# Optimization experiments

Hardware: AMD Instinct MI355X
Metric: run time of the kernel (lower is better)

## Reference

```python
import jax, jax.numpy as jnp
import numpy as np

D_MODEL = 512
NHEAD = 8


def setup_inputs() -> dict:
    key = jax.random.key(0)
    k0, k1, k2 = jax.random.split(key, 3)
    s = 1.0 / np.sqrt(D_MODEL)  # torch default uniform init bound (xavier-ish)
    return {
        "x": jax.random.normal(k0, (2, 4096, D_MODEL), dtype=jnp.float32),
        "in_proj_w": jax.random.uniform(k1, (3 * D_MODEL, D_MODEL), jnp.float32, -s, s),
        "in_proj_b": jnp.zeros((3 * D_MODEL,), jnp.float32),
        "out_proj_w": jax.random.uniform(k2, (D_MODEL, D_MODEL), jnp.float32, -s, s),
        "out_proj_b": jnp.zeros((D_MODEL,), jnp.float32),
        "window_size": 128,
    }


def reference(x, in_proj_w, in_proj_b, out_proj_w, out_proj_b, window_size):
    # Faithful to nn.MultiheadAttention (eval mode, dropout inactive).
    # NOTE: PyTorch bool attn_mask: True = disallowed. The module sets True
    # INSIDE the window, so in-window positions are masked OUT.
    B, S, D = x.shape
    H = NHEAD
    hd = D // H

    qkv = x @ in_proj_w.T + in_proj_b                      # [B,S,3D]
    q, k, v = jnp.split(qkv, 3, axis=-1)
    q = q.reshape(B, S, H, hd).transpose(0, 2, 1, 3)       # [B,H,S,hd]
    k = k.reshape(B, S, H, hd).transpose(0, 2, 1, 3)
    v = v.reshape(B, S, H, hd).transpose(0, 2, 1, 3)

    scores = jnp.einsum('bhqd,bhkd->bhqk', q, k) / jnp.sqrt(jnp.float32(hd))

    idx = jnp.arange(S)
    in_window = jnp.abs(idx[:, None] - idx[None, :]) <= window_size  # [S,S]
    scores = jnp.where(in_window, -jnp.inf, scores)

    attn = jax.nn.softmax(scores, axis=-1)                 # [B,H,S,S]
    ctx = jnp.einsum('bhqk,bhkd->bhqd', attn, v)           # [B,H,S,hd]
    ctx = ctx.transpose(0, 2, 1, 3).reshape(B, S, D)       # [B,S,D]
    return ctx @ out_proj_w.T + out_proj_b
```

## Files before the change

kernel.cpp:

```cpp
#include <hip/hip_runtime.h>
#include <hip/hip_bf16.h>

typedef unsigned short u16;
typedef __bf16 bf16x8 __attribute__((ext_vector_type(8)));
typedef float f32x4 __attribute__((ext_vector_type(4)));

__device__ __forceinline__ f32x4 mfma16(bf16x8 a, bf16x8 b, f32x4 c) {
    return __builtin_amdgcn_mfma_f32_16x16x32_bf16(a, b, c, 0, 0, 0);
}

__device__ __forceinline__ u16 f2b(float x) {
    union { float f; unsigned u; } a; a.f = x;
    unsigned r = a.u + 0x7fffu + ((a.u >> 16) & 1u);
    return (u16)(r >> 16);
}
__device__ __forceinline__ unsigned f2b2(float a, float b) {
    union { __hip_bfloat162 h; unsigned u; } cv;
    cv.h = __float22bfloat162_rn(make_float2(a, b));
    return cv.u;
}
__device__ __forceinline__ void async16(const u16* g, u16* l) {
    __builtin_amdgcn_global_load_lds((const __attribute__((address_space(1))) unsigned int*)g,
                                     (__attribute__((address_space(3))) unsigned int*)l, 16, 0, 0);
}

#define NX  (8192 * 512)
#define NWQ (1536 * 512)
#define NWO (512 * 512)
__global__ __launch_bounds__(256) void k_cast_all(const float* __restrict__ x,
                                                  const float* __restrict__ wq,
                                                  const float* __restrict__ wo,
                                                  u16* __restrict__ xb,
                                                  u16* __restrict__ wqb,
                                                  u16* __restrict__ wob) {
    int i = (blockIdx.x * 256 + threadIdx.x) * 4;
    const float* s; u16* d; int off;
    if (i < NX)            { s = x;  d = xb;  off = i; }
    else if (i < NX + NWQ) { s = wq; d = wqb; off = i - NX; }
    else                   { s = wo; d = wob; off = i - NX - NWQ; }
    float4 f = *(const float4*)&s[off];
    uint2 o = make_uint2(f2b2(f.x, f.y), f2b2(f.z, f.w));
    *(uint2*)&d[off] = o;
}

__global__ __launch_bounds__(256, 3) void k_gemm_qkv(const u16* __restrict__ xb,
                                                     const u16* __restrict__ wb,
                                                     const float* __restrict__ bias,
                                                     u16* __restrict__ qkvout) {
    __shared__ u16 AL[2][4096];
    __shared__ u16 WL[2][4096];
    const int tid = threadIdx.x;
    const int w = tid >> 6, lane = tid & 63, l15 = lane & 15, quad = lane >> 4;
    const int mb = blockIdx.x * 128, nb = blockIdx.y * 128;

    f32x4 acc[2][8];
#pragma unroll
    for (int i = 0; i < 2; i++)
#pragma unroll
        for (int j = 0; j < 8; j++) acc[i][j] = (f32x4){0.f, 0.f, 0.f, 0.f};

    const u16* agp = xb + (size_t)(mb + w * 32 + (lane >> 2)) * 512 + (lane & 3) * 8;
    const u16* wgp = wb + (size_t)(nb + w * 32 + (lane >> 2)) * 512 + (lane & 3) * 8;
    const int ldst = w * 1024 + lane * 8;

    async16(agp, &AL[0][ldst]);
    async16(agp + 16 * 512, &AL[0][ldst + 512]);
    async16(wgp, &WL[0][ldst]);
    async16(wgp + 16 * 512, &WL[0][ldst + 512]);
    __syncthreads();
    int p = 0;
    for (int ks = 0; ks < 16; ks++) {
        if (ks < 15) {
            int k0n = (ks + 1) * 32;
            async16(agp + k0n, &AL[p ^ 1][ldst]);
            async16(agp + 16 * 512 + k0n, &AL[p ^ 1][ldst + 512]);
            async16(wgp + k0n, &WL[p ^ 1][ldst]);
            async16(wgp + 16 * 512 + k0n, &WL[p ^ 1][ldst + 512]);
        }
        bf16x8 a0 = *(const bf16x8*)&AL[p][(w * 32 + l15) * 32 + quad * 8];
        bf16x8 a1 = *(const bf16x8*)&AL[p][(w * 32 + 16 + l15) * 32 + quad * 8];
#pragma unroll
        for (int nt = 0; nt < 8; nt++) {
            bf16x8 bfr = *(const bf16x8*)&WL[p][(nt * 16 + l15) * 32 + quad * 8];
            acc[0][nt] = mfma16(a0, bfr, acc[0][nt]);
            acc[1][nt] = mfma16(a1, bfr, acc[1][nt]);
        }
        if (ks < 15) { __syncthreads(); p ^= 1; }
    }
    const int seg = nb >> 9;
    u16* obase = qkvout + (size_t)seg * (16ull * 4096 * 64);
    if (seg == 0) {
        const float sc = 0.125f * 1.44269504088896340736f;
#pragma unroll
        for (int mt = 0; mt < 2; mt++)
#pragma unroll
            for (int nt = 0; nt < 8; nt++) {
                int dcol = nb + nt * 16 + l15;
                int hh = (dcol >> 6) & 7, dloc = dcol & 63;
                float bs = bias[dcol];
#pragma unroll
                for (int r = 0; r < 4; r++) {
                    int m = mb + w * 32 + mt * 16 + quad * 4 + r;
                    float vv = (acc[mt][nt][r] + bs) * sc;
                    int b = m >> 12, s = m & 4095;
                    obase[((size_t)((b * 8 + hh) * 4096 + s)) * 64 + dloc] = f2b(vv);
                }
            }
    } else if (seg == 1) {
#pragma unroll
        for (int mt = 0; mt < 2; mt++)
#pragma unroll
            for (int nt = 0; nt < 8; nt++) {
                int dcol = nb + nt * 16 + l15;
                int hh = (dcol >> 6) & 7, d = dcol & 63;
                int h2 = d >> 5, qk = (d >> 3) & 3, j = d & 7;
                float bs = bias[dcol];
                int m0 = mb + w * 32 + mt * 16 + quad * 4;
                int b = m0 >> 12, s0 = m0 & 4095;
                int kt = s0 >> 6, ksx = s0 & 63;
                int kg2 = ksx >> 5, rem = ksx & 31;
                int t2 = (rem >> 2) & 1, lb = (rem >> 3) * 4;
                size_t base = ((((((size_t)(b * 8 + hh) * 64 + kt) * 2 + kg2) * 2 + t2) * 2 + h2) * 4 + qk) * 16 + lb;
#pragma unroll
                for (int r = 0; r < 4; r++)
                    obase[(base + r) * 8 + j] = f2b(acc[mt][nt][r] + bs);
            }
    } else {
#pragma unroll
        for (int mt = 0; mt < 2; mt++)
#pragma unroll
            for (int nt = 0; nt < 8; nt++) {
                int c = nb + nt * 16 + l15;
                int hh = (c >> 6) & 7, d = c & 63;
                int mbv = d >> 4, l15v = d & 15;
                float bs = bias[c];
                int m0 = mb + w * 32 + mt * 16 + quad * 4;
                int b = m0 >> 12, si = m0 & 4095;
                int kt = si >> 6, ksx = si & 63;
                int kg2 = ksx >> 5, qv = (ksx >> 3) & 3, j0 = ksx & 7;
                uint2 o = make_uint2(f2b2(acc[mt][nt][0] + bs, acc[mt][nt][1] + bs),
                                     f2b2(acc[mt][nt][2] + bs, acc[mt][nt][3] + bs));
                size_t F = (((((size_t)(b * 8 + hh) * 64 + kt) * 2 + kg2) * 4 + mbv) * 4 + qv) * 16 + l15v;
                *(uint2*)&obase[F * 8 + j0] = o;
            }
    }
}

__global__ __launch_bounds__(256, 2) void k_attn(const u16* __restrict__ qg,
                                                 const u16* __restrict__ kfg,
                                                 const u16* __restrict__ vfg,
                                                 u16* __restrict__ ctx,
                                                 const int* __restrict__ win) {
    __shared__ u16 KL[2][4096];
    __shared__ u16 VL[2][4096];
    const int tid = threadIdx.x;
    const int w = tid >> 6, lane = tid & 63, l15 = lane & 15, quad = lane >> 4;
    const int bh = blockIdx.y;
    const int qb0 = blockIdx.x * 128;
    const int qb0w = qb0 + w * 32;
    const int W = win[0];
    const size_t bhb = (size_t)bh * 4096 * 64;

    bf16x8 qf[2][2];
#pragma unroll
    for (int g = 0; g < 2; g++) {
        const u16* qrow = &qg[bhb + (size_t)(qb0w + g * 16 + l15) * 64];
        qf[g][0] = *(const bf16x8*)&qrow[quad * 8];
        qf[g][1] = *(const bf16x8*)&qrow[32 + quad * 8];
    }
    bf16x8 ones8;
    {
        u16 v = (l15 == 0) ? (u16)0x3F80 : (u16)0;
        union { u16 a[8]; bf16x8 b; } c;
#pragma unroll
        for (int i = 0; i < 8; i++) c.a[i] = v;
        ones8 = c.b;
    }

    f32x4 O[2][4];
#pragma unroll
    for (int g = 0; g < 2; g++)
#pragma unroll
        for (int mb = 0; mb < 4; mb++) O[g][mb] = (f32x4){0.f, 0.f, 0.f, 0.f};
    f32x4 O1[2] = {(f32x4){0.f, 0.f, 0.f, 0.f}, (f32x4){0.f, 0.f, 0.f, 0.f}};

    const u16* kbase = kfg + bhb;
    const u16* vbase = vfg + bhb;
    const int soff = w * 1024 + lane * 8;

    auto skip = [&](int kb) { return max(qb0 + 127 - kb, kb + 63 - qb0) <= W; };
    int kb = 0;
    while (kb < 4096 && skip(kb)) kb += 64;
    {
        const u16* kt_p = kbase + (size_t)(kb >> 6) * 4096;
        const u16* vt_p = vbase + (size_t)(kb >> 6) * 4096;
        async16(kt_p + soff, &KL[0][soff]);
        async16(kt_p + soff + 512, &KL[0][soff + 512]);
        async16(vt_p + soff, &VL[0][soff]);
        async16(vt_p + soff + 512, &VL[0][soff + 512]);
    }
    __syncthreads();
    int p = 0;
    while (kb < 4096) {
        int kb_next = kb + 64;
        while (kb_next < 4096 && skip(kb_next)) kb_next += 64;
        if (kb_next < 4096) {
            const u16* kt_p = kbase + (size_t)(kb_next >> 6) * 4096;
            const u16* vt_p = vbase + (size_t)(kb_next >> 6) * 4096;
            async16(kt_p + soff, &KL[p ^ 1][soff]);
            async16(kt_p + soff + 512, &KL[p ^ 1][soff + 512]);
            async16(vt_p + soff, &VL[p ^ 1][soff]);
            async16(vt_p + soff + 512, &VL[p ^ 1][soff + 512]);
        }
        const bool partial = (kb + 63 >= qb0 - W) && (kb <= qb0 + 127 + W);
        bf16x8 kf[2][2][2];
#pragma unroll
        for (int kg = 0; kg < 2; kg++)
#pragma unroll
            for (int t = 0; t < 2; t++)
#pragma unroll
                for (int h = 0; h < 2; h++)
                    kf[kg][t][h] = *(const bf16x8*)&KL[p][((((kg * 2 + t) * 2 + h) * 4 + quad) * 16 + l15) * 8];
        bf16x8 vfr[2][4];
#pragma unroll
        for (int kg = 0; kg < 2; kg++)
#pragma unroll
            for (int mb = 0; mb < 4; mb++)
                vfr[kg][mb] = *(const bf16x8*)&VL[p][(((kg * 4 + mb) * 4 + quad) * 16 + l15) * 8];

        f32x4 C[2][2][2];
#pragma unroll
        for (int g = 0; g < 2; g++)
#pragma unroll
            for (int kg = 0; kg < 2; kg++)
#pragma unroll
                for (int t = 0; t < 2; t++) {
                    f32x4 z = (f32x4){0.f, 0.f, 0.f, 0.f};
                    C[g][kg][t] = mfma16(kf[kg][t][0], qf[g][0], z);
                    C[g][kg][t] = mfma16(kf[kg][t][1], qf[g][1], C[g][kg][t]);
                }
        bf16x8 pb[2][2];
        if (!partial) {
#pragma unroll
            for (int g = 0; g < 2; g++)
#pragma unroll
                for (int kg = 0; kg < 2; kg++) {
                    float p0 = __builtin_amdgcn_exp2f(C[g][kg][0][0]);
                    float p1 = __builtin_amdgcn_exp2f(C[g][kg][0][1]);
                    float p2 = __builtin_amdgcn_exp2f(C[g][kg][0][2]);
                    float p3 = __builtin_amdgcn_exp2f(C[g][kg][0][3]);
                    float p4 = __builtin_amdgcn_exp2f(C[g][kg][1][0]);
                    float p5 = __builtin_amdgcn_exp2f(C[g][kg][1][1]);
                    float p6 = __builtin_amdgcn_exp2f(C[g][kg][1][2]);
                    float p7 = __builtin_amdgcn_exp2f(C[g][kg][1][3]);
                    union { uint4 u; bf16x8 v; } pk;
                    pk.u = make_uint4(f2b2(p0, p1), f2b2(p2, p3), f2b2(p4, p5), f2b2(p6, p7));
                    pb[g][kg] = pk.v;
                }
        } else {
#pragma unroll
            for (int g = 0; g < 2; g++) {
                int qr = qb0w + g * 16 + l15;
#pragma unroll
                for (int kg = 0; kg < 2; kg++) {
                    float pv[8];
#pragma unroll
                    for (int t = 0; t < 2; t++)
#pragma unroll
                        for (int r = 0; r < 4; r++) {
                            int key = kb + kg * 32 + 8 * quad + 4 * t + r;
                            int dd = qr - key; dd = dd < 0 ? -dd : dd;
                            pv[t * 4 + r] = (dd <= W) ? 0.f
                                          : __builtin_amdgcn_exp2f(C[g][kg][t][r]);
                        }
                    union { uint4 u; bf16x8 v; } pk;
                    pk.u = make_uint4(f2b2(pv[0], pv[1]), f2b2(pv[2], pv[3]),
                                      f2b2(pv[4], pv[5]), f2b2(pv[6], pv[7]));
                    pb[g][kg] = pk.v;
                }
            }
        }
#pragma unroll
        for (int kg = 0; kg < 2; kg++)
#pragma unroll
            for (int g = 0; g < 2; g++) {
#pragma unroll
                for (int mb = 0; mb < 4; mb++)
                    O[g][mb] = mfma16(vfr[kg][mb], pb[g][kg], O[g][mb]);
                O1[g] = mfma16(ones8, pb[g][kg], O1[g]);
            }
        if (kb_next < 4096) { __syncthreads(); p ^= 1; }
        kb = kb_next;
    }
    int b = bh >> 3, h = bh & 7;
#pragma unroll
    for (int g = 0; g < 2; g++) {
        float ls = __shfl(O1[g][0], l15);
        float inv = 1.0f / ls;
        int qr = qb0w + g * 16 + l15;
        size_t rowoff = ((size_t)(b * 4096 + qr)) * 512 + h * 64;
#pragma unroll
        for (int mb = 0; mb < 4; mb++) {
            uint2 o = make_uint2(f2b2(O[g][mb][0] * inv, O[g][mb][1] * inv),
                                 f2b2(O[g][mb][2] * inv, O[g][mb][3] * inv));
            *(uint2*)&ctx[rowoff + mb * 16 + quad * 4] = o;
        }
    }
}

__global__ __launch_bounds__(256, 2) void k_gemm_out(const u16* __restrict__ ab,
                                                     const u16* __restrict__ wb,
                                                     const float* __restrict__ bias,
                                                     float* __restrict__ out) {
    __shared__ u16 AL[2][4096];
    __shared__ u16 WL[2][2048];
    const int tid = threadIdx.x;
    const int w = tid >> 6, lane = tid & 63, l15 = lane & 15, quad = lane >> 4;
    const int mb = blockIdx.x * 128, nb = blockIdx.y * 64;

    f32x4 acc[2][4];
#pragma unroll
    for (int i = 0; i < 2; i++)
#pragma unroll
        for (int j = 0; j < 4; j++) acc[i][j] = (f32x4){0.f, 0.f, 0.f, 0.f};

    const u16* agp = ab + (size_t)(mb + w * 32 + (lane >> 2)) * 512 + (lane & 3) * 8;
    const u16* wgp = wb + (size_t)(nb + w * 16 + (lane >> 2)) * 512 + (lane & 3) * 8;
    const int ldstA = w * 1024 + lane * 8;
    const int ldstW = w * 512 + lane * 8;

    async16(agp, &AL[0][ldstA]);
    async16(agp + 16 * 512, &AL[0][ldstA + 512]);
    async16(wgp, &WL[0][ldstW]);
    __syncthreads();
    int p = 0;
    for (int ks = 0; ks < 16; ks++) {
        if (ks < 15) {
            int k0n = (ks + 1) * 32;
            async16(agp + k0n, &AL[p ^ 1][ldstA]);
            async16(agp + 16 * 512 + k0n, &AL[p ^ 1][ldstA + 512]);
            async16(wgp + k0n, &WL[p ^ 1][ldstW]);
        }
        bf16x8 a0 = *(const bf16x8*)&AL[p][(w * 32 + l15) * 32 + quad * 8];
        bf16x8 a1 = *(const bf16x8*)&AL[p][(w * 32 + 16 + l15) * 32 + quad * 8];
#pragma unroll
        for (int nt = 0; nt < 4; nt++) {
            bf16x8 bfr = *(const bf16x8*)&WL[p][(nt * 16 + l15) * 32 + quad * 8];
            acc[0][nt] = mfma16(a0, bfr, acc[0][nt]);
            acc[1][nt] = mfma16(a1, bfr, acc[1][nt]);
        }
        if (ks < 15) { __syncthreads(); p ^= 1; }
    }
#pragma unroll
    for (int mt = 0; mt < 2; mt++)
#pragma unroll
        for (int nt = 0; nt < 4; nt++) {
            int n = nb + nt * 16 + l15;
            float bs = bias[n];
#pragma unroll
            for (int r = 0; r < 4; r++) {
                int m = mb + w * 32 + mt * 16 + quad * 4 + r;
                out[(size_t)m * 512 + n] = acc[mt][nt][r] + bs;
            }
        }
}

extern "C" void kernel_launch(void* const* d_in, const int* in_sizes, int n_in,
                              void* d_out, int out_size, void* d_ws, size_t ws_size,
                              hipStream_t stream) {
    const float* x    = (const float*)d_in[0];
    const float* wqkv = (const float*)d_in[1];
    const float* bqkv = (const float*)d_in[2];
    const float* wout = (const float*)d_in[3];
    const float* bout = (const float*)d_in[4];
    const int*   win  = (const int*)d_in[5];
    float* out = (float*)d_out;

    u16* xb    = (u16*)d_ws;
    u16* wqkvb = xb    + 8192ull * 512;
    u16* woutb = wqkvb + 1536ull * 512;
    u16* qkvb  = woutb + 512ull * 512;
    u16* ctxb  = qkvb  + 3ull * 16 * 4096 * 64;

    k_cast_all<<<5120, 256, 0, stream>>>(x, wqkv, wout, xb, wqkvb, woutb);
    k_gemm_qkv<<<dim3(64, 12), 256, 0, stream>>>(xb, wqkvb, bqkv, qkvb);
    k_attn<<<dim3(32, 16), 256, 0, stream>>>(qkvb, qkvb + 16ull * 4096 * 64,
                                             qkvb + 32ull * 4096 * 64, ctxb, win);
    k_gemm_out<<<dim3(64, 8), 256, 0, stream>>>(ctxb, woutb, bout, out);
}
```

Before: 198.7 us.

## Use single-wave attention blocks with register-prefetched V and LDS-staged K

The attention kernel now launches one 64-thread wave per block, each handling 32 query rows, instead of four waves sharing a 128-row block. This removes block-wide barriers. K tiles are double-buffered in LDS through async loads, while V fragments are prefetched straight into registers for the next tile, with an explicit waitcnt standing in for __syncthreads. The tighter per-wave skip window lets each wave skip more fully masked tiles. In exchange, each K/V tile is loaded four times as often, raising global/L2 traffic, and register pressure goes up from the V prefetch.

```diff
diff --git a/kernel.cpp b/kernel.cpp
--- a/kernel.cpp
+++ b/kernel.cpp
@@ -146,25 +146,23 @@
     }
 }
 
-__global__ __launch_bounds__(256, 2) void k_attn(const u16* __restrict__ qg,
-                                                 const u16* __restrict__ kfg,
-                                                 const u16* __restrict__ vfg,
-                                                 u16* __restrict__ ctx,
-                                                 const int* __restrict__ win) {
-    __shared__ u16 KL[2][4096];
-    __shared__ u16 VL[2][4096];
-    const int tid = threadIdx.x;
-    const int w = tid >> 6, lane = tid & 63, l15 = lane & 15, quad = lane >> 4;
+__global__ __launch_bounds__(64, 2) void k_attn(const u16* __restrict__ qg,
+                                                const u16* __restrict__ kfg,
+                                                const u16* __restrict__ vfg,
+                                                u16* __restrict__ ctx,
+                                                const int* __restrict__ win) {
+    __shared__ u16 KP[2][4096];
+    const int lane = threadIdx.x & 63;
+    const int l15 = lane & 15, quad = lane >> 4;
     const int bh = blockIdx.y;
-    const int qb0 = blockIdx.x * 128;
-    const int qb0w = qb0 + w * 32;
+    const int qb0 = blockIdx.x * 32;
     const int W = win[0];
     const size_t bhb = (size_t)bh * 4096 * 64;
 
     bf16x8 qf[2][2];
 #pragma unroll
     for (int g = 0; g < 2; g++) {
-        const u16* qrow = &qg[bhb + (size_t)(qb0w + g * 16 + l15) * 64];
+        const u16* qrow = &qg[bhb + (size_t)(qb0 + g * 16 + l15) * 64];
         qf[g][0] = *(const bf16x8*)&qrow[quad * 8];
         qf[g][1] = *(const bf16x8*)&qrow[32 + quad * 8];
     }
@@ -184,35 +182,28 @@
         for (int mb = 0; mb < 4; mb++) O[g][mb] = (f32x4){0.f, 0.f, 0.f, 0.f};
     f32x4 O1[2] = {(f32x4){0.f, 0.f, 0.f, 0.f}, (f32x4){0.f, 0.f, 0.f, 0.f}};
 
-    const u16* kbase = kfg + bhb;
-    const u16* vbase = vfg + bhb;
-    const int soff = w * 1024 + lane * 8;
-
-    auto skip = [&](int kb) { return max(qb0 + 127 - kb, kb + 63 - qb0) <= W; };
-    int kb = 0;
-    while (kb < 4096 && skip(kb)) kb += 64;
+    const u16* kbase = kfg + bhb + lane * 8;
+    const u16* vbase = vfg + bhb + lane * 8;
+
+    auto skip = [&](int kb) { return max(qb0 + 31 - kb, kb + 63 - qb0) <= W; };
+    auto nextk = [&](int kb) { while (kb < 4096 && skip(kb)) kb += 64; return kb; };
+
+    bf16x8 vn[8];
+    int kb = nextk(0);
     {
-        const u16* kt_p = kbase + (size_t)(kb >> 6) * 4096;
-        const u16* vt_p = vbase + (size_t)(kb >> 6) * 4096;
-        async16(kt_p + soff, &KL[0][soff]);
-        async16(kt_p + soff + 512, &KL[0][soff + 512]);
-        async16(vt_p + soff, &VL[0][soff]);
-        async16(vt_p + soff + 512, &VL[0][soff + 512]);
-    }
-    __syncthreads();
+        const u16* kp = kbase + (size_t)(kb >> 6) * 4096;
+        const u16* vp = vbase + (size_t)(kb >> 6) * 4096;
+#pragma unroll
+        for (int i = 0; i < 8; i++) async16(kp + i * 512, &KP[0][i * 512 + lane * 8]);
+#pragma unroll
+        for (int f = 0; f < 8; f++) vn[f] = *(const bf16x8*)(vp + f * 512);
+    }
     int p = 0;
     while (kb < 4096) {
-        int kb_next = kb + 64;
-        while (kb_next < 4096 && skip(kb_next)) kb_next += 64;
-        if (kb_next < 4096) {
-            const u16* kt_p = kbase + (size_t)(kb_next >> 6) * 4096;
-            const u16* vt_p = vbase + (size_t)(kb_next >> 6) * 4096;
-            async16(kt_p + soff, &KL[p ^ 1][soff]);
-            async16(kt_p + soff + 512, &KL[p ^ 1][soff + 512]);
-            async16(vt_p + soff, &VL[p ^ 1][soff]);
-            async16(vt_p + soff + 512, &VL[p ^ 1][soff + 512]);
-        }
-        const bool partial = (kb + 63 >= qb0 - W) && (kb <= qb0 + 127 + W);
+        __builtin_amdgcn_s_waitcnt(0x0F70);
+        bf16x8 vc[8];
+#pragma unroll
+        for (int f = 0; f < 8; f++) vc[f] = vn[f];
         bf16x8 kf[2][2][2];
 #pragma unroll
         for (int kg = 0; kg < 2; kg++)
@@ -220,14 +211,17 @@
             for (int t = 0; t < 2; t++)
 #pragma unroll
                 for (int h = 0; h < 2; h++)
-                    kf[kg][t][h] = *(const bf16x8*)&KL[p][((((kg * 2 + t) * 2 + h) * 4 + quad) * 16 + l15) * 8];
-        bf16x8 vfr[2][4];
-#pragma unroll
-        for (int kg = 0; kg < 2; kg++)
-#pragma unroll
-            for (int mb = 0; mb < 4; mb++)
-                vfr[kg][mb] = *(const bf16x8*)&VL[p][(((kg * 4 + mb) * 4 + quad) * 16 + l15) * 8];
-
+                    kf[kg][t][h] = *(const bf16x8*)&KP[p][((((kg * 2 + t) * 2 + h) * 4 + quad) * 16 + l15) * 8];
+        int kn = nextk(kb + 64);
+        if (kn < 4096) {
+            const u16* kp = kbase + (size_t)(kn >> 6) * 4096;
+            const u16* vp = vbase + (size_t)(kn >> 6) * 4096;
+#pragma unroll
+            for (int i = 0; i < 8; i++) async16(kp + i * 512, &KP[p ^ 1][i * 512 + lane * 8]);
+#pragma unroll
+            for (int f = 0; f < 8; f++) vn[f] = *(const bf16x8*)(vp + f * 512);
+        }
+        const bool partial = (kb + 63 >= qb0 - W) && (kb <= qb0 + 31 + W);
         f32x4 C[2][2][2];
 #pragma unroll
         for (int g = 0; g < 2; g++)
@@ -260,7 +254,7 @@
         } else {
 #pragma unroll
             for (int g = 0; g < 2; g++) {
-                int qr = qb0w + g * 16 + l15;
+                int qr = qb0 + g * 16 + l15;
 #pragma unroll
                 for (int kg = 0; kg < 2; kg++) {
                     float pv[8];
@@ -286,18 +280,18 @@
             for (int g = 0; g < 2; g++) {
 #pragma unroll
                 for (int mb = 0; mb < 4; mb++)
-                    O[g][mb] = mfma16(vfr[kg][mb], pb[g][kg], O[g][mb]);
+                    O[g][mb] = mfma16(vc[kg * 4 + mb], pb[g][kg], O[g][mb]);
                 O1[g] = mfma16(ones8, pb[g][kg], O1[g]);
             }
-        if (kb_next < 4096) { __syncthreads(); p ^= 1; }
-        kb = kb_next;
+        p ^= 1;
+        kb = kn;
     }
     int b = bh >> 3, h = bh & 7;
 #pragma unroll
     for (int g = 0; g < 2; g++) {
         float ls = __shfl(O1[g][0], l15);
         float inv = 1.0f / ls;
-        int qr = qb0w + g * 16 + l15;
+        int qr = qb0 + g * 16 + l15;
         size_t rowoff = ((size_t)(b * 4096 + qr)) * 512 + h * 64;
 #pragma unroll
         for (int mb = 0; mb < 4; mb++) {
@@ -384,7 +378,7 @@
 
     k_cast_all<<<5120, 256, 0, stream>>>(x, wqkv, wout, xb, wqkvb, woutb);
     k_gemm_qkv<<<dim3(64, 12), 256, 0, stream>>>(xb, wqkvb, bqkv, qkvb);
-    k_attn<<<dim3(32, 16), 256, 0, stream>>>(qkvb, qkvb + 16ull * 4096 * 64,
+    k_attn<<<dim3(128, 16), 64, 0, stream>>>(qkvb, qkvb + 16ull * 4096 * 64,
                                              qkvb + 32ull * 4096 * 64, ctxb, win);
     k_gemm_out<<<dim3(64, 8), 256, 0, stream>>>(ctxb, woutb, bout, out);
 }
```

Result: slower. 213.5 us (+7.5%).

## Split attention key range across two wave groups per block and merge partials

Applied to the files above, without the earlier changes.

The attention kernel now launches 512 threads per block. Two groups of four waves each process half of the non-skipped key tiles for the same 128-query block, each with its own double-buffered LDS staging. At the end, group 1 writes its partial output and row sums to shared memory and group 0 adds them and normalizes. The aim is more parallelism on the serial key loop, since the grid of only 512 blocks underfills the GPU. The cost is doubled LDS, an extra reduction through shared memory, and block-wide barriers that now also wait on the other group.

```diff
diff --git a/kernel.cpp b/kernel.cpp
--- a/kernel.cpp
+++ b/kernel.cpp
@@ -146,15 +146,16 @@
     }
 }
 
-__global__ __launch_bounds__(256, 2) void k_attn(const u16* __restrict__ qg,
+__global__ __launch_bounds__(512, 4) void k_attn(const u16* __restrict__ qg,
                                                  const u16* __restrict__ kfg,
                                                  const u16* __restrict__ vfg,
                                                  u16* __restrict__ ctx,
                                                  const int* __restrict__ win) {
-    __shared__ u16 KL[2][4096];
-    __shared__ u16 VL[2][4096];
+    __shared__ u16 KL[2][2][4096];
+    __shared__ u16 VL[2][2][4096];
     const int tid = threadIdx.x;
-    const int w = tid >> 6, lane = tid & 63, l15 = lane & 15, quad = lane >> 4;
+    const int wid = tid >> 6, grp = wid >> 2, w = wid & 3;
+    const int lane = tid & 63, l15 = lane & 15, quad = lane >> 4;
     const int bh = blockIdx.y;
     const int qb0 = blockIdx.x * 128;
     const int qb0w = qb0 + w * 32;
@@ -186,124 +187,153 @@
 
     const u16* kbase = kfg + bhb;
     const u16* vbase = vfg + bhb;
-    const int soff = w * 1024 + lane * 8;
-
-    auto skip = [&](int kb) { return max(qb0 + 127 - kb, kb + 63 - qb0) <= W; };
-    int kb = 0;
-    while (kb < 4096 && skip(kb)) kb += 64;
-    {
-        const u16* kt_p = kbase + (size_t)(kb >> 6) * 4096;
-        const u16* vt_p = vbase + (size_t)(kb >> 6) * 4096;
-        async16(kt_p + soff, &KL[0][soff]);
-        async16(kt_p + soff + 512, &KL[0][soff + 512]);
-        async16(vt_p + soff, &VL[0][soff]);
-        async16(vt_p + soff + 512, &VL[0][soff + 512]);
-    }
+    const int tidg = tid & 255;
+    const int soff = (tidg >> 6) * 1024 + lane * 8;
+
+    int a = qb0 + 127 - W;
+    int T_lo = (a <= 0) ? 0 : ((a + 63) >> 6);
+    int b2 = qb0 + W - 63;
+    int T_hi = (b2 < 0) ? -1 : (b2 >> 6);
+    if (T_hi > 63) T_hi = 63;
+    if (T_lo > 63) T_lo = 64;
+    int cnt = T_hi - T_lo + 1; if (cnt < 0) cnt = 0;
+    const int nvalid = 64 - cnt;
+    const int n0 = (nvalid + 1) >> 1, n1 = nvalid - n0;
+    const int base = grp ? n0 : 0;
+    const int mycnt = grp ? n1 : n0;
+    auto tileof = [&](int idx) { return ((idx < T_lo) ? idx : idx + cnt) << 6; };
+    auto stage = [&](int idx, int buf) {
+        int kt = tileof(idx) >> 6;
+        const u16* kt_p = kbase + (size_t)kt * 4096;
+        const u16* vt_p = vbase + (size_t)kt * 4096;
+        async16(kt_p + soff, &KL[grp][buf][soff]);
+        async16(kt_p + soff + 512, &KL[grp][buf][soff + 512]);
+        async16(vt_p + soff, &VL[grp][buf][soff]);
+        async16(vt_p + soff + 512, &VL[grp][buf][soff + 512]);
+    };
+
+    if (mycnt > 0) stage(base, 0);
     __syncthreads();
     int p = 0;
-    while (kb < 4096) {
-        int kb_next = kb + 64;
-        while (kb_next < 4096 && skip(kb_next)) kb_next += 64;
-        if (kb_next < 4096) {
-            const u16* kt_p = kbase + (size_t)(kb_next >> 6) * 4096;
-            const u16* vt_p = vbase + (size_t)(kb_next >> 6) * 4096;
-            async16(kt_p + soff, &KL[p ^ 1][soff]);
-            async16(kt_p + soff + 512, &KL[p ^ 1][soff + 512]);
-            async16(vt_p + soff, &VL[p ^ 1][soff]);
-            async16(vt_p + soff + 512, &VL[p ^ 1][soff + 512]);
-        }
-        const bool partial = (kb + 63 >= qb0 - W) && (kb <= qb0 + 127 + W);
-        bf16x8 kf[2][2][2];
-#pragma unroll
-        for (int kg = 0; kg < 2; kg++)
-#pragma unroll
-            for (int t = 0; t < 2; t++)
-#pragma unroll
-                for (int h = 0; h < 2; h++)
-                    kf[kg][t][h] = *(const bf16x8*)&KL[p][((((kg * 2 + t) * 2 + h) * 4 + quad) * 16 + l15) * 8];
-        bf16x8 vfr[2][4];
-#pragma unroll
-        for (int kg = 0; kg < 2; kg++)
+    for (int i = 0; i < n0; i++) {
+        if (i + 1 < mycnt) stage(base + i + 1, p ^ 1);
+        if (i < mycnt) {
+            const int kb = tileof(base + i);
+            const bool partial = (kb + 63 >= qb0 - W) && (kb <= qb0 + 127 + W);
+            bf16x8 kf[2][2][2];
+#pragma unroll
+            for (int kg = 0; kg < 2; kg++)
+#pragma unroll
+                for (int t = 0; t < 2; t++)
+#pragma unroll
+                    for (int h = 0; h < 2; h++)
+                        kf[kg][t][h] = *(const bf16x8*)&KL[grp][p][((((kg * 2 + t) * 2 + h) * 4 + quad) * 16 + l15) * 8];
+            bf16x8 vfr[2][4];
+#pragma unroll
+            for (int kg = 0; kg < 2; kg++)
+#pragma unroll
+                for (int mb = 0; mb < 4; mb++)
+                    vfr[kg][mb] = *(const bf16x8*)&VL[grp][p][(((kg * 4 + mb) * 4 + quad) * 16 + l15) * 8];
+
+            f32x4 C[2][2][2];
+#pragma unroll
+            for (int g = 0; g < 2; g++)
+#pragma unroll
+                for (int kg = 0; kg < 2; kg++)
+#pragma unroll
+                    for (int t = 0; t < 2; t++) {
+                        f32x4 z = (f32x4){0.f, 0.f, 0.f, 0.f};
+                        C[g][kg][t] = mfma16(kf[kg][t][0], qf[g][0], z);
+                        C[g][kg][t] = mfma16(kf[kg][t][1], qf[g][1], C[g][kg][t]);
+                    }
+            bf16x8 pb[2][2];
+            if (!partial) {
+#pragma unroll
+                for (int g = 0; g < 2; g++)
+#pragma unroll
+                    for (int kg = 0; kg < 2; kg++) {
+                        float p0 = __builtin_amdgcn_exp2f(C[g][kg][0][0]);
+                        float p1 = __builtin_amdgcn_exp2f(C[g][kg][0][1]);
+                        float p2 = __builtin_amdgcn_exp2f(C[g][kg][0][2]);
+                        float p3 = __builtin_amdgcn_exp2f(C[g][kg][0][3]);
+                        float p4 = __builtin_amdgcn_exp2f(C[g][kg][1][0]);
+                        float p5 = __builtin_amdgcn_exp2f(C[g][kg][1][1]);
+                        float p6 = __builtin_amdgcn_exp2f(C[g][kg][1][2]);
+                        float p7 = __builtin_amdgcn_exp2f(C[g][kg][1][3]);
+                        union { uint4 u; bf16x8 v; } pk;
+                        pk.u = make_uint4(f2b2(p0, p1), f2b2(p2, p3), f2b2(p4, p5), f2b2(p6, p7));
+                        pb[g][kg] = pk.v;
+                    }
+            } else {
+#pragma unroll
+                for (int g = 0; g < 2; g++) {
+                    int qr = qb0w + g * 16 + l15;
+#pragma unroll
+                    for (int kg = 0; kg < 2; kg++) {
+                        float pv[8];
+#pragma unroll
+                        for (int t = 0; t < 2; t++)
+#pragma unroll
+                            for (int r = 0; r < 4; r++) {
+                                int key = kb + kg * 32 + 8 * quad + 4 * t + r;
+                                int dd = qr - key; dd = dd < 0 ? -dd : dd;
+                                pv[t * 4 + r] = (dd <= W) ? 0.f
+                                              : __builtin_amdgcn_exp2f(C[g][kg][t][r]);
+                            }
+                        union { uint4 u; bf16x8 v; } pk;
+                        pk.u = make_uint4(f2b2(pv[0], pv[1]), f2b2(pv[2], pv[3]),
+                                          f2b2(pv[4], pv[5]), f2b2(pv[6], pv[7]));
+                        pb[g][kg] = pk.v;
+                    }
+                }
+            }
+#pragma unroll
+            for (int kg = 0; kg < 2; kg++)
+#pragma unroll
+                for (int g = 0; g < 2; g++) {
+#pragma unroll
+                    for (int mb = 0; mb < 4; mb++)
+                        O[g][mb] = mfma16(vfr[kg][mb], pb[g][kg], O[g][mb]);
+                    O1[g] = mfma16(ones8, pb[g][kg], O1[g]);
+                }
+        }
+        __syncthreads();
+        p ^= 1;
+    }
+    float* mO = (float*)&KL[0][0][0];
+    float* mL = (float*)&VL[0][0][0];
+    if (grp == 1) {
+#pragma unroll
+        for (int g = 0; g < 2; g++) {
 #pragma unroll
             for (int mb = 0; mb < 4; mb++)
-                vfr[kg][mb] = *(const bf16x8*)&VL[p][(((kg * 4 + mb) * 4 + quad) * 16 + l15) * 8];
-
-        f32x4 C[2][2][2];
-#pragma unroll
-        for (int g = 0; g < 2; g++)
-#pragma unroll
-            for (int kg = 0; kg < 2; kg++)
-#pragma unroll
-                for (int t = 0; t < 2; t++) {
-                    f32x4 z = (f32x4){0.f, 0.f, 0.f, 0.f};
-                    C[g][kg][t] = mfma16(kf[kg][t][0], qf[g][0], z);
-                    C[g][kg][t] = mfma16(kf[kg][t][1], qf[g][1], C[g][kg][t]);
-                }
-        bf16x8 pb[2][2];
-        if (!partial) {
-#pragma unroll
-            for (int g = 0; g < 2; g++)
-#pragma unroll
-                for (int kg = 0; kg < 2; kg++) {
-                    float p0 = __builtin_amdgcn_exp2f(C[g][kg][0][0]);
-                    float p1 = __builtin_amdgcn_exp2f(C[g][kg][0][1]);
-                    float p2 = __builtin_amdgcn_exp2f(C[g][kg][0][2]);
-                    float p3 = __builtin_amdgcn_exp2f(C[g][kg][0][3]);
-                    float p4 = __builtin_amdgcn_exp2f(C[g][kg][1][0]);
-                    float p5 = __builtin_amdgcn_exp2f(C[g][kg][1][1]);
-                    float p6 = __builtin_amdgcn_exp2f(C[g][kg][1][2]);
-                    float p7 = __builtin_amdgcn_exp2f(C[g][kg][1][3]);
-                    union { uint4 u; bf16x8 v; } pk;
-                    pk.u = make_uint4(f2b2(p0, p1), f2b2(p2, p3), f2b2(p4, p5), f2b2(p6, p7));
-                    pb[g][kg] = pk.v;
-                }
-        } else {
-#pragma unroll
-            for (int g = 0; g < 2; g++) {
-                int qr = qb0w + g * 16 + l15;
-#pragma unroll
-                for (int kg = 0; kg < 2; kg++) {
-                    float pv[8];
-#pragma unroll
-                    for (int t = 0; t < 2; t++)
-#pragma unroll
-                        for (int r = 0; r < 4; r++) {
-                            int key = kb + kg * 32 + 8 * quad + 4 * t + r;
-                            int dd = qr - key; dd = dd < 0 ? -dd : dd;
-                            pv[t * 4 + r] = (dd <= W) ? 0.f
-                                          : __builtin_amdgcn_exp2f(C[g][kg][t][r]);
-                        }
-                    union { uint4 u; bf16x8 v; } pk;
-                    pk.u = make_uint4(f2b2(pv[0], pv[1]), f2b2(pv[2], pv[3]),
-                                      f2b2(pv[4], pv[5]), f2b2(pv[6], pv[7]));
-                    pb[g][kg] = pk.v;
-                }
-            }
-        }
-#pragma unroll
-        for (int kg = 0; kg < 2; kg++)
-#pragma unroll
-            for (int g = 0; g < 2; g++) {
-#pragma unroll
-                for (int mb = 0; mb < 4; mb++)
-                    O[g][mb] = mfma16(vfr[kg][mb], pb[g][kg], O[g][mb]);
-                O1[g] = mfma16(ones8, pb[g][kg], O1[g]);
-            }
-        if (kb_next < 4096) { __syncthreads(); p ^= 1; }
-        kb = kb_next;
-    }
-    int b = bh >> 3, h = bh & 7;
-#pragma unroll
-    for (int g = 0; g < 2; g++) {
-        float ls = __shfl(O1[g][0], l15);
-        float inv = 1.0f / ls;
-        int qr = qb0w + g * 16 + l15;
-        size_t rowoff = ((size_t)(b * 4096 + qr)) * 512 + h * 64;
-#pragma unroll
-        for (int mb = 0; mb < 4; mb++) {
-            uint2 o = make_uint2(f2b2(O[g][mb][0] * inv, O[g][mb][1] * inv),
-                                 f2b2(O[g][mb][2] * inv, O[g][mb][3] * inv));
-            *(uint2*)&ctx[rowoff + mb * 16 + quad * 4] = o;
+#pragma unroll
+                for (int r = 0; r < 4; r++)
+                    mO[((w * 2 + g) * 16 + mb * 4 + r) * 64 + lane] = O[g][mb][r];
+            mL[(w * 2 + g) * 64 + lane] = O1[g][0];
+        }
+    }
+    __syncthreads();
+    if (grp == 0) {
+        int b = bh >> 3, h = bh & 7;
+#pragma unroll
+        for (int g = 0; g < 2; g++) {
+#pragma unroll
+            for (int mb = 0; mb < 4; mb++)
+#pragma unroll
+                for (int r = 0; r < 4; r++)
+                    O[g][mb][r] += mO[((w * 2 + g) * 16 + mb * 4 + r) * 64 + lane];
+            float lsg = O1[g][0] + mL[(w * 2 + g) * 64 + lane];
+            float ls = __shfl(lsg, l15);
+            float inv = 1.0f / ls;
+            int qr = qb0w + g * 16 + l15;
+            size_t rowoff = ((size_t)(b * 4096 + qr)) * 512 + h * 64;
+#pragma unroll
+            for (int mb = 0; mb < 4; mb++) {
+                uint2 o = make_uint2(f2b2(O[g][mb][0] * inv, O[g][mb][1] * inv),
+                                     f2b2(O[g][mb][2] * inv, O[g][mb][3] * inv));
+                *(uint2*)&ctx[rowoff + mb * 16 + quad * 4] = o;
+            }
         }
     }
 }
@@ -384,7 +414,7 @@
 
     k_cast_all<<<5120, 256, 0, stream>>>(x, wqkv, wout, xb, wqkvb, woutb);
     k_gemm_qkv<<<dim3(64, 12), 256, 0, stream>>>(xb, wqkvb, bqkv, qkvb);
-    k_attn<<<dim3(32, 16), 256, 0, stream>>>(qkvb, qkvb + 16ull * 4096 * 64,
+    k_attn<<<dim3(32, 16), 512, 0, stream>>>(qkvb, qkvb + 16ull * 4096 * 64,
                                              qkvb + 32ull * 4096 * 64, ctxb, win);
     k_gemm_out<<<dim3(64, 8), 256, 0, stream>>>(ctxb, woutb, bout, out);
 }
```

After: 345.5 us. 1.74x slower.

## Split attention key range across two blocks and merge partial results

Applied to the files above, without the earlier changes.

The attention grid gains a z dimension of two, and each block handles half of the non-skipped key tiles, which it finds by closed-form tile indexing instead of a skip loop. Unnormalized bf16 partial contexts and row sums are written to workspace, and a new merge kernel adds them and normalizes. This doubles the number of blocks (512 up to 1024) to fill more of the GPU, and the launch-bounds occupancy hint rises from 2 to 4. The cost is an extra kernel launch, extra workspace traffic, and a second bf16 rounding of the unnormalized partials. Softmax is not max-subtracted, so this relies on the scores being small enough for exp2 to stay in range.

```diff
diff --git a/kernel.cpp b/kernel.cpp
--- a/kernel.cpp
+++ b/kernel.cpp
@@ -18,6 +18,9 @@
     union { __hip_bfloat162 h; unsigned u; } cv;
     cv.h = __float22bfloat162_rn(make_float2(a, b));
     return cv.u;
+}
+__device__ __forceinline__ float b2f(u16 x) {
+    union { unsigned u; float f; } a; a.u = ((unsigned)x) << 16; return a.f;
 }
 __device__ __forceinline__ void async16(const u16* g, u16* l) {
     __builtin_amdgcn_global_load_lds((const __attribute__((address_space(1))) unsigned int*)g,
@@ -146,16 +149,18 @@
     }
 }
 
-__global__ __launch_bounds__(256, 2) void k_attn(const u16* __restrict__ qg,
+__global__ __launch_bounds__(256, 4) void k_attn(const u16* __restrict__ qg,
                                                  const u16* __restrict__ kfg,
                                                  const u16* __restrict__ vfg,
-                                                 u16* __restrict__ ctx,
+                                                 u16* __restrict__ ctxp,
+                                                 float* __restrict__ lsp,
                                                  const int* __restrict__ win) {
     __shared__ u16 KL[2][4096];
     __shared__ u16 VL[2][4096];
     const int tid = threadIdx.x;
     const int w = tid >> 6, lane = tid & 63, l15 = lane & 15, quad = lane >> 4;
     const int bh = blockIdx.y;
+    const int z = blockIdx.z;
     const int qb0 = blockIdx.x * 128;
     const int qb0w = qb0 + w * 32;
     const int W = win[0];
@@ -188,30 +193,34 @@
     const u16* vbase = vfg + bhb;
     const int soff = w * 1024 + lane * 8;
 
-    auto skip = [&](int kb) { return max(qb0 + 127 - kb, kb + 63 - qb0) <= W; };
-    int kb = 0;
-    while (kb < 4096 && skip(kb)) kb += 64;
-    {
-        const u16* kt_p = kbase + (size_t)(kb >> 6) * 4096;
-        const u16* vt_p = vbase + (size_t)(kb >> 6) * 4096;
-        async16(kt_p + soff, &KL[0][soff]);
-        async16(kt_p + soff + 512, &KL[0][soff + 512]);
-        async16(vt_p + soff, &VL[0][soff]);
-        async16(vt_p + soff + 512, &VL[0][soff + 512]);
-    }
+    int a = qb0 + 127 - W;
+    int T_lo = (a <= 0) ? 0 : ((a + 63) >> 6);
+    int b2 = qb0 + W - 63;
+    int T_hi = (b2 < 0) ? -1 : (b2 >> 6);
+    if (T_hi > 63) T_hi = 63;
+    if (T_lo > 63) T_lo = 64;
+    int cnt = T_hi - T_lo + 1; if (cnt < 0) cnt = 0;
+    const int nvalid = 64 - cnt;
+    const int n0 = (nvalid + 1) >> 1;
+    const int base = z ? n0 : 0;
+    const int mycnt = z ? (nvalid - n0) : n0;
+    auto tileof = [&](int idx) { return ((idx < T_lo) ? idx : idx + cnt) << 6; };
+    auto stage = [&](int idx, int buf) {
+        int kt = tileof(idx) >> 6;
+        const u16* kt_p = kbase + (size_t)kt * 4096;
+        const u16* vt_p = vbase + (size_t)kt * 4096;
+        async16(kt_p + soff, &KL[buf][soff]);
+        async16(kt_p + soff + 512, &KL[buf][soff + 512]);
+        async16(vt_p + soff, &VL[buf][soff]);
+        async16(vt_p + soff + 512, &VL[buf][soff + 512]);
+    };
+
+    if (mycnt > 0) stage(base, 0);
     __syncthreads();
     int p = 0;
-    while (kb < 4096) {
-        int kb_next = kb + 64;
-        while (kb_next < 4096 && skip(kb_next)) kb_next += 64;
-        if (kb_next < 4096) {
-            const u16* kt_p = kbase + (size_t)(kb_next >> 6) * 4096;
-            const u16* vt_p = vbase + (size_t)(kb_next >> 6) * 4096;
-            async16(kt_p + soff, &KL[p ^ 1][soff]);
-            async16(kt_p + soff + 512, &KL[p ^ 1][soff + 512]);
-            async16(vt_p + soff, &VL[p ^ 1][soff]);
-            async16(vt_p + soff + 512, &VL[p ^ 1][soff + 512]);
-        }
+    for (int i = 0; i < mycnt; i++) {
+        if (i + 1 < mycnt) stage(base + i + 1, p ^ 1);
+        const int kb = tileof(base + i);
         const bool partial = (kb + 63 >= qb0 - W) && (kb <= qb0 + 127 + W);
         bf16x8 kf[2][2][2];
 #pragma unroll
@@ -235,8 +244,8 @@
             for (int kg = 0; kg < 2; kg++)
 #pragma unroll
                 for (int t = 0; t < 2; t++) {
-                    f32x4 z = (f32x4){0.f, 0.f, 0.f, 0.f};
-                    C[g][kg][t] = mfma16(kf[kg][t][0], qf[g][0], z);
+                    f32x4 zz = (f32x4){0.f, 0.f, 0.f, 0.f};
+                    C[g][kg][t] = mfma16(kf[kg][t][0], qf[g][0], zz);
                     C[g][kg][t] = mfma16(kf[kg][t][1], qf[g][1], C[g][kg][t]);
                 }
         bf16x8 pb[2][2];
@@ -289,23 +298,45 @@
                     O[g][mb] = mfma16(vfr[kg][mb], pb[g][kg], O[g][mb]);
                 O1[g] = mfma16(ones8, pb[g][kg], O1[g]);
             }
-        if (kb_next < 4096) { __syncthreads(); p ^= 1; }
-        kb = kb_next;
-    }
+        if (i + 1 < mycnt) { __syncthreads(); p ^= 1; }
+    }
+    u16* cp = ctxp + (size_t)z * (2ull * 4096 * 512);
+    float* lp = lsp + (size_t)z * (16 * 4096);
     int b = bh >> 3, h = bh & 7;
 #pragma unroll
     for (int g = 0; g < 2; g++) {
-        float ls = __shfl(O1[g][0], l15);
-        float inv = 1.0f / ls;
         int qr = qb0w + g * 16 + l15;
+        if (quad == 0) lp[bh * 4096 + qr] = O1[g][0];
         size_t rowoff = ((size_t)(b * 4096 + qr)) * 512 + h * 64;
 #pragma unroll
         for (int mb = 0; mb < 4; mb++) {
-            uint2 o = make_uint2(f2b2(O[g][mb][0] * inv, O[g][mb][1] * inv),
-                                 f2b2(O[g][mb][2] * inv, O[g][mb][3] * inv));
-            *(uint2*)&ctx[rowoff + mb * 16 + quad * 4] = o;
-        }
-    }
+            uint2 o = make_uint2(f2b2(O[g][mb][0], O[g][mb][1]),
+                                 f2b2(O[g][mb][2], O[g][mb][3]));
+            *(uint2*)&cp[rowoff + mb * 16 + quad * 4] = o;
+        }
+    }
+}
+
+__global__ __launch_bounds__(256) void k_merge(const u16* __restrict__ c0,
+                                               const float* __restrict__ l0,
+                                               u16* __restrict__ ctx) {
+    const u16* c1 = c0 + 2ull * 4096 * 512;
+    const float* l1 = l0 + 16 * 4096;
+    int t = blockIdx.x * 256 + threadIdx.x;
+    int e = t * 8;
+    int b = e >> 21, rem = e & ((1 << 21) - 1);
+    int s = rem >> 9, hd = rem & 511, h = hd >> 6;
+    int bh = b * 8 + h;
+    float inv = 1.0f / (l0[bh * 4096 + s] + l1[bh * 4096 + s]);
+    uint4 a = *(const uint4*)&c0[e];
+    uint4 bb = *(const uint4*)&c1[e];
+    const u16* pa = (const u16*)&a;
+    const u16* pbt = (const u16*)&bb;
+    u16 o[8];
+#pragma unroll
+    for (int i = 0; i < 8; i++)
+        o[i] = f2b((b2f(pa[i]) + b2f(pbt[i])) * inv);
+    *(uint4*)&ctx[e] = *(uint4*)o;
 }
 
 __global__ __launch_bounds__(256, 2) void k_gemm_out(const u16* __restrict__ ab,
@@ -381,10 +412,14 @@
     u16* woutb = wqkvb + 1536ull * 512;
     u16* qkvb  = woutb + 512ull * 512;
     u16* ctxb  = qkvb  + 3ull * 16 * 4096 * 64;
+    u16* ctx01 = ctxb  + 2ull * 4096 * 512;
+    float* ls01 = (float*)(ctx01 + 2ull * 2 * 4096 * 512);
 
     k_cast_all<<<5120, 256, 0, stream>>>(x, wqkv, wout, xb, wqkvb, woutb);
     k_gemm_qkv<<<dim3(64, 12), 256, 0, stream>>>(xb, wqkvb, bqkv, qkvb);
-    k_attn<<<dim3(32, 16), 256, 0, stream>>>(qkvb, qkvb + 16ull * 4096 * 64,
-                                             qkvb + 32ull * 4096 * 64, ctxb, win);
+    k_attn<<<dim3(32, 16, 2), 256, 0, stream>>>(qkvb, qkvb + 16ull * 4096 * 64,
+                                                qkvb + 32ull * 4096 * 64,
+                                                ctx01, ls01, win);
+    k_merge<<<2048, 256, 0, stream>>>(ctx01, ls01, ctxb);
     k_gemm_out<<<dim3(64, 8), 256, 0, stream>>>(ctxb, woutb, bout, out);
 }
```

New measurement: 371.0 us. 1.87x slower.
